# Performance work log

Hardware: AMD Instinct MI355X
Metric: run time of the kernel (lower is better)

Reference implementation:

```python
import jax, jax.numpy as jnp
import numpy as np

NUM_HEADS = 16
HEAD_SIZE = 64
EMB = NUM_HEADS * HEAD_SIZE
B, S = 2, 2048


def setup_inputs() -> dict:
    key = jax.random.key(0)
    ks = jax.random.split(key, 8)
    return {
        "values": jax.random.normal(ks[0], (B, S, EMB), dtype=jnp.float32),
        "keys": jax.random.normal(ks[1], (B, S, EMB), dtype=jnp.float32),
        "queries": jax.random.normal(ks[2], (B, S, EMB), dtype=jnp.float32),
        "mask": jnp.ones((B, 1, 1, S), dtype=jnp.int32),
        "Wq": jax.random.normal(ks[3], (HEAD_SIZE, HEAD_SIZE), dtype=jnp.float32) / np.sqrt(HEAD_SIZE),
        "Wk": jax.random.normal(ks[4], (HEAD_SIZE, HEAD_SIZE), dtype=jnp.float32) / np.sqrt(HEAD_SIZE),
        "Wv": jax.random.normal(ks[5], (HEAD_SIZE, HEAD_SIZE), dtype=jnp.float32) / np.sqrt(HEAD_SIZE),
        "Wout": jax.random.normal(ks[6], (EMB, EMB), dtype=jnp.float32) / np.sqrt(EMB),
        "bout": jax.random.normal(ks[7], (EMB,), dtype=jnp.float32) * 0.01,
    }


def reference(values, keys, queries, mask, Wq, Wk, Wv, Wout, bout):
    n, q_len, E = queries.shape
    H, D = NUM_HEADS, HEAD_SIZE
    # split heads: [n, len, H, D]
    v = values.reshape(n, -1, H, D)
    k = keys.reshape(n, -1, H, D)
    q = queries.reshape(n, q_len, H, D)
    # per-head shared linears (torch Linear: x @ W.T), no bias
    v = jnp.einsum("nkhd,cd->nkhc", v, Wv)
    k = jnp.einsum("nkhd,cd->nkhc", k, Wk)
    q = jnp.einsum("nqhd,cd->nqhc", q, Wq)
    # scores: [n, H, q, k]
    energy = jnp.einsum("nqhd,nkhd->nhqk", q, k)
    energy = jnp.where(mask == 0, jnp.float32(-1e28), energy)
    # NOTE: source scales by sqrt(embedding_size), not head_size
    attn = jax.nn.softmax(energy / jnp.sqrt(jnp.float32(E)), axis=3)
    out = jnp.einsum("nhqk,nkhd->nqhd", attn, v).reshape(n, q_len, E)
    return out @ Wout.T + bout
```

## Files before the change

### kernel.cpp

```cpp
#include <hip/hip_runtime.h>
#include <hip/hip_bf16.h>


#define NHB 16
#define HS  64
#define EMB 1024
#define BB  2
#define SS  2048
#define NT  (SS / 64)

typedef __bf16 bf16_t;
typedef bf16_t bf16x8 __attribute__((ext_vector_type(8)));
typedef bf16_t bf16x4 __attribute__((ext_vector_type(4)));
typedef float  f32x4  __attribute__((ext_vector_type(4)));

__device__ __forceinline__ f32x4 mfma16(bf16x8 a, bf16x8 b, f32x4 c) {
    return __builtin_amdgcn_mfma_f32_16x16x32_bf16(a, b, c, 0, 0, 0);
}

__device__ __forceinline__ float fast_exp2(float x) {
#if __has_builtin(__builtin_amdgcn_exp2f)
    return __builtin_amdgcn_exp2f(x);
#else
    float r;
    asm("v_exp_f32 %0, %1" : "=v"(r) : "v"(x));
    return r;
#endif
}

__global__ __launch_bounds__(512) void proj_kernel(
    const float* __restrict__ queries, const float* __restrict__ keys,
    const float* __restrict__ values,
    const float* __restrict__ Wq, const float* __restrict__ Wk,
    const float* __restrict__ Wv,
    bf16_t* __restrict__ Qb, bf16_t* __restrict__ Kb, bf16_t* __restrict__ Vt)
{
    __shared__ bf16_t Ws[3][64][72];
    __shared__ bf16_t Xs[128][72];

    const int tid  = threadIdx.x;
    const int wave = tid >> 6, lane = tid & 63;
    const int q4 = lane >> 4, l16 = lane & 15;
    const int s0 = blockIdx.x * 128;
    const int h  = blockIdx.y, n = blockIdx.z;

    #pragma unroll
    for (int i = 0; i < 6; ++i) {
        int g = i * 512 + tid;
        int mW = g >> 10;
        int idx4 = g & 1023;
        const float* wp = (mW == 0) ? Wq : (mW == 1) ? Wk : Wv;
        float4 v = ((const float4*)wp)[idx4];
        int r = idx4 >> 4, c = (idx4 & 15) * 4;
        Ws[mW][r][c+0] = (bf16_t)v.x; Ws[mW][r][c+1] = (bf16_t)v.y;
        Ws[mW][r][c+2] = (bf16_t)v.z; Ws[mW][r][c+3] = (bf16_t)v.w;
    }

    const size_t headBase = (size_t)(n * NHB + h) * SS * HS;

    float4 gx[4];
    auto loadX = [&](const float* xp) {
        #pragma unroll
        for (int i = 0; i < 4; ++i) {
            int idx4 = i * 512 + tid;
            int r = idx4 >> 4, c = (idx4 & 15) * 4;
            gx[i] = *(const float4*)&xp[((size_t)(n * SS + s0 + r)) * EMB + h * HS + c];
        }
    };
    loadX(queries);

    for (int p = 0; p < 3; ++p) {
        __syncthreads();
        #pragma unroll
        for (int i = 0; i < 4; ++i) {
            int idx4 = i * 512 + tid;
            int r = idx4 >> 4, c = (idx4 & 15) * 4;
            Xs[r][c+0] = (bf16_t)gx[i].x; Xs[r][c+1] = (bf16_t)gx[i].y;
            Xs[r][c+2] = (bf16_t)gx[i].z; Xs[r][c+3] = (bf16_t)gx[i].w;
        }
        if (p == 0) loadX(keys);
        else if (p == 1) loadX(values);
        __syncthreads();

        bf16x8 xf[2], wf[4][2];
        #pragma unroll
        for (int kk = 0; kk < 2; ++kk)
            xf[kk] = *(const bf16x8*)&Xs[wave * 16 + l16][kk * 32 + q4 * 8];
        #pragma unroll
        for (int ct = 0; ct < 4; ++ct)
            #pragma unroll
            for (int kk = 0; kk < 2; ++kk)
                wf[ct][kk] = *(const bf16x8*)&Ws[p][ct * 16 + l16][kk * 32 + q4 * 8];

        if (p < 2) {
            bf16_t* dst = (p == 0) ? Qb : Kb;
            const float sc = (p == 0) ? (0.03125f * 1.44269504f) : 1.0f;
            bf16x8 lo, hi;
            #pragma unroll
            for (int ct = 0; ct < 4; ++ct) {
                f32x4 acc = {};
                acc = mfma16(wf[ct][0], xf[0], acc);
                acc = mfma16(wf[ct][1], xf[1], acc);
                #pragma unroll
                for (int i = 0; i < 4; ++i) {
                    bf16_t v = (bf16_t)(acc[i] * sc);
                    if (ct < 2) lo[ct * 4 + i] = v;
                    else        hi[(ct - 2) * 4 + i] = v;
                }
            }
            bf16_t* rp = dst + headBase
                + (size_t)(s0 + wave * 16 + l16) * HS + q4 * 16;
            *(bf16x8*)rp = lo;
            *(bf16x8*)(rp + 8) = hi;
        } else {
            #pragma unroll
            for (int ct = 0; ct < 4; ++ct) {
                f32x4 acc = {};
                acc = mfma16(xf[0], wf[ct][0], acc);
                acc = mfma16(xf[1], wf[ct][1], acc);
                bf16x4 pk;
                #pragma unroll
                for (int i = 0; i < 4; ++i) pk[i] = (bf16_t)acc[i];
                *(bf16x4*)&Vt[headBase + (size_t)(ct * 16 + l16) * SS
                              + s0 + (wave >> 1) * 32 + q4 * 8 + (wave & 1) * 4] = pk;
            }
        }
    }
}

__global__ __launch_bounds__(512) void attn_kernel(
    const bf16_t* __restrict__ Qb, const bf16_t* __restrict__ Kb,
    const bf16_t* __restrict__ Vt, const int* __restrict__ mask,
    bf16_t* __restrict__ Og)
{
    __shared__ __align__(16) unsigned char smem[37376];
    auto Ks = (bf16_t(*)[64][72])(smem);
    auto Vs = (bf16_t(*)[64][72])(smem + 18432);
    auto Ms = (float(*)[64])(smem + 36864);
    float* fbuf = (float*)smem;
    float* lbuf = (float*)(smem + 32768);

    const int tid = threadIdx.x;
    const int w = tid >> 6, lane = tid & 63;
    const int q4 = lane >> 4, l16 = lane & 15;
    const int wq = w & 3, wk = w >> 2;
    const int qt = blockIdx.x, h = blockIdx.y, n = blockIdx.z;
    const size_t headBase = (size_t)(n * NHB + h) * SS * HS;
    const int* mrow = mask + n * SS;

    const int sr = tid >> 3, sc = (tid & 7) * 8;
    const bf16_t* kb_src = Kb + headBase + (size_t)sr * HS + sc;
    const bf16_t* vt_src = Vt + headBase + (size_t)sr * SS + sc;

    bf16x8 bq[2][2];
    #pragma unroll
    for (int st = 0; st < 2; ++st) {
        const bf16_t* qptr = Qb + headBase
            + (size_t)(qt * 128 + wq * 32 + st * 16 + l16) * HS;
        bq[st][0] = *(const bf16x8*)&qptr[q4 * 8];
        bq[st][1] = *(const bf16x8*)&qptr[32 + q4 * 8];
    }

    bf16x8 ones;
    #pragma unroll
    for (int i = 0; i < 8; ++i) ones[i] = (bf16_t)1.0f;

    f32x4 oaccT[2][4] = {};
    f32x4 lacc[2] = {};

    *(bf16x8*)&Ks[0][sr][sc] = *(const bf16x8*)kb_src;
    *(bf16x8*)&Vs[0][sr][sc] = *(const bf16x8*)vt_src;
    if (tid < 64) Ms[0][tid] = mrow[tid] ? 0.0f : -3e38f;
    __syncthreads();

    for (int kt = 0; kt < NT; ++kt) {
        const int cur = kt & 1;
        const bool has_next = (kt + 1) < NT;
        bf16x8 gk, gv; float gm = 0.f;
        if (has_next) {
            const int k0n = (kt + 1) * 64;
            gk = *(const bf16x8*)(kb_src + (size_t)k0n * HS);
            gv = *(const bf16x8*)(vt_src + k0n);
            if (tid < 64) gm = mrow[k0n + tid] ? 0.0f : -3e38f;
        }

        f32x4 sacc[2][2];
        #pragma unroll
        for (int c2 = 0; c2 < 2; ++c2) {
            const int ct = wk * 2 + c2;
            float4 bias = *(const float4*)&Ms[cur][ct * 16 + q4 * 4];
            f32x4 b4 = {bias.x, bias.y, bias.z, bias.w};
            sacc[0][c2] = b4; sacc[1][c2] = b4;
            bf16x8 ak0 = *(const bf16x8*)&Ks[cur][ct * 16 + l16][q4 * 8];
            bf16x8 ak1 = *(const bf16x8*)&Ks[cur][ct * 16 + l16][32 + q4 * 8];
            #pragma unroll
            for (int st = 0; st < 2; ++st) {
                sacc[st][c2] = mfma16(ak0, bq[st][0], sacc[st][c2]);
                sacc[st][c2] = mfma16(ak1, bq[st][1], sacc[st][c2]);
            }
        }

        bf16x4 pv[2][2];
        #pragma unroll
        for (int c2 = 0; c2 < 2; ++c2)
            #pragma unroll
            for (int st = 0; st < 2; ++st) {
                bf16x4 pk;
                #pragma unroll
                for (int j = 0; j < 4; ++j)
                    pk[j] = (bf16_t)fast_exp2(sacc[st][c2][j]);
                pv[st][c2] = pk;
            }

        bf16x8 pa[2];
        #pragma unroll
        for (int st = 0; st < 2; ++st)
            pa[st] = __builtin_shufflevector(pv[st][0], pv[st][1],
                                             0, 1, 2, 3, 4, 5, 6, 7);
        #pragma unroll
        for (int dt = 0; dt < 4; ++dt) {
            bf16x8 av = *(const bf16x8*)&Vs[cur][dt * 16 + l16][wk * 32 + q4 * 8];
            oaccT[0][dt] = mfma16(av, pa[0], oaccT[0][dt]);
            oaccT[1][dt] = mfma16(av, pa[1], oaccT[1][dt]);
        }
        lacc[0] = mfma16(ones, pa[0], lacc[0]);
        lacc[1] = mfma16(ones, pa[1], lacc[1]);

        if (has_next) {
            const int nxt = 1 - cur;
            *(bf16x8*)&Ks[nxt][sr][sc] = gk;
            *(bf16x8*)&Vs[nxt][sr][sc] = gv;
            if (tid < 64) Ms[nxt][tid] = gm;
        }
        __syncthreads();
    }

    float ls[2] = {lacc[0][0], lacc[1][0]};

    if (w >= 4) {
        const int lanecol = wq * 64 + lane;
        #pragma unroll
        for (int st = 0; st < 2; ++st) {
            #pragma unroll
            for (int dt = 0; dt < 4; ++dt)
                #pragma unroll
                for (int j = 0; j < 4; ++j)
                    fbuf[(st * 16 + dt * 4 + j) * 256 + lanecol] = oaccT[st][dt][j];
            lbuf[st * 256 + lanecol] = ls[st];
        }
    }
    __syncthreads();
    if (w < 4) {
        const int lanecol = wq * 64 + lane;
        #pragma unroll
        for (int st = 0; st < 2; ++st) {
            #pragma unroll
            for (int dt = 0; dt < 4; ++dt)
                #pragma unroll
                for (int j = 0; j < 4; ++j)
                    oaccT[st][dt][j] += fbuf[(st * 16 + dt * 4 + j) * 256 + lanecol];
            ls[st] += lbuf[st * 256 + lanecol];
        }
        #pragma unroll
        for (int st = 0; st < 2; ++st) {
            const float inv = 1.f / ls[st];
            const int qrow = qt * 128 + wq * 32 + st * 16 + l16;
            bf16_t* obase = Og + ((size_t)(n * SS + qrow)) * EMB + h * HS;
            #pragma unroll
            for (int dt = 0; dt < 4; ++dt) {
                bf16x4 ov;
                #pragma unroll
                for (int j = 0; j < 4; ++j) ov[j] = (bf16_t)(oaccT[st][dt][j] * inv);
                *(bf16x4*)&obase[dt * 16 + q4 * 4] = ov;
            }
        }
    }
}

__global__ __launch_bounds__(512) void outproj_kernel(
    const bf16_t* __restrict__ Og, const float* __restrict__ Wout,
    const float* __restrict__ bout, float* __restrict__ out)
{
    __shared__ bf16_t As[2][128][72];
    __shared__ bf16_t Bs[2][64][72];
    const int tid = threadIdx.x;
    const int w = tid >> 6, lane = tid & 63;
    const int q4 = lane >> 4, l16 = lane & 15;
    const int wr = w >> 1, wc = w & 1;
    const int t0 = blockIdx.x * 128, c0 = blockIdx.y * 64;

    const int sr0 = tid >> 3, sc0 = (tid & 7) * 8;
    const int sr1 = sr0 + 64;
    const bf16_t* a0 = Og + (size_t)(t0 + sr0) * EMB + sc0;
    const bf16_t* a1 = Og + (size_t)(t0 + sr1) * EMB + sc0;
    const float*  b0 = Wout + (size_t)(c0 + sr0) * EMB + sc0;

    auto cvt8 = [](float4 x, float4 y) {
        bf16x8 r;
        r[0] = (bf16_t)x.x; r[1] = (bf16_t)x.y; r[2] = (bf16_t)x.z; r[3] = (bf16_t)x.w;
        r[4] = (bf16_t)y.x; r[5] = (bf16_t)y.y; r[6] = (bf16_t)y.z; r[7] = (bf16_t)y.w;
        return r;
    };

    f32x4 acc[2][2] = {};

    *(bf16x8*)&As[0][sr0][sc0] = *(const bf16x8*)a0;
    *(bf16x8*)&As[0][sr1][sc0] = *(const bf16x8*)a1;
    *(bf16x8*)&Bs[0][sr0][sc0] = cvt8(*(const float4*)b0, *(const float4*)(b0 + 4));
    __syncthreads();

    const int NE = EMB / 64;
    for (int et = 0; et < NE; ++et) {
        const int cur = et & 1;
        const bool has_next = (et + 1) < NE;
        bf16x8 ga0, ga1; float4 gb0, gb1;
        if (has_next) {
            const int e0 = (et + 1) * 64;
            ga0 = *(const bf16x8*)(a0 + e0); ga1 = *(const bf16x8*)(a1 + e0);
            gb0 = *(const float4*)(b0 + e0); gb1 = *(const float4*)(b0 + e0 + 4);
        }

        bf16x8 af[2][2], bfr[2][2];
        #pragma unroll
        for (int st = 0; st < 2; ++st)
            #pragma unroll
            for (int kk = 0; kk < 2; ++kk)
                af[st][kk] = *(const bf16x8*)&As[cur][wr * 32 + st * 16 + l16][kk * 32 + q4 * 8];
        #pragma unroll
        for (int ct = 0; ct < 2; ++ct)
            #pragma unroll
            for (int kk = 0; kk < 2; ++kk)
                bfr[ct][kk] = *(const bf16x8*)&Bs[cur][wc * 32 + ct * 16 + l16][kk * 32 + q4 * 8];
        #pragma unroll
        for (int st = 0; st < 2; ++st)
            #pragma unroll
            for (int ct = 0; ct < 2; ++ct) {
                acc[st][ct] = mfma16(af[st][0], bfr[ct][0], acc[st][ct]);
                acc[st][ct] = mfma16(af[st][1], bfr[ct][1], acc[st][ct]);
            }

        if (has_next) {
            const int nxt = 1 - cur;
            *(bf16x8*)&As[nxt][sr0][sc0] = ga0;
            *(bf16x8*)&As[nxt][sr1][sc0] = ga1;
            *(bf16x8*)&Bs[nxt][sr0][sc0] = cvt8(gb0, gb1);
        }
        __syncthreads();
    }

    #pragma unroll
    for (int ct = 0; ct < 2; ++ct) {
        const int c = c0 + wc * 32 + ct * 16 + l16;
        const float bias = bout[c];
        #pragma unroll
        for (int st = 0; st < 2; ++st)
            #pragma unroll
            for (int i = 0; i < 4; ++i)
                out[(size_t)(t0 + wr * 32 + st * 16 + q4 * 4 + i) * EMB + c]
                    = acc[st][ct][i] + bias;
    }
}

extern "C" void kernel_launch(void* const* d_in, const int* in_sizes, int n_in,
                              void* d_out, int out_size, void* d_ws, size_t ws_size,
                              hipStream_t stream)
{
    const float* values  = (const float*)d_in[0];
    const float* keys    = (const float*)d_in[1];
    const float* queries = (const float*)d_in[2];
    const int*   mask    = (const int*)d_in[3];
    const float* Wq      = (const float*)d_in[4];
    const float* Wk      = (const float*)d_in[5];
    const float* Wv      = (const float*)d_in[6];
    const float* Wout    = (const float*)d_in[7];
    const float* bout    = (const float*)d_in[8];
    float* out = (float*)d_out;

    const size_t M8 = 8ull * 1024 * 1024;
    bf16_t* Qb = (bf16_t*)d_ws;
    bf16_t* Kb = (bf16_t*)((char*)d_ws + 1 * M8);
    bf16_t* Vt = (bf16_t*)((char*)d_ws + 2 * M8);
    bf16_t* Og = (bf16_t*)((char*)d_ws + 3 * M8);

    proj_kernel<<<dim3(SS / 128, NHB, BB), 512, 0, stream>>>(
        queries, keys, values, Wq, Wk, Wv, Qb, Kb, Vt);
    attn_kernel<<<dim3(SS / 128, NHB, BB), 512, 0, stream>>>(
        Qb, Kb, Vt, mask, Og);
    outproj_kernel<<<dim3((BB * SS) / 128, EMB / 64), 512, 0, stream>>>(
        Og, Wout, bout, out);
}
```

Baseline: 169.1 us.

## Load projection inputs directly to registers and pre-convert Wout for wider out-projection tiles

The projection kernel now loads each wave's Q/K/V input rows straight into MFMA fragment registers as bf16, which removes the shared-memory staging buffer and its per-pass barriers. A separate kernel converts Wout to bf16 once into workspace that aliases the Qb buffer, which is already consumed by then. The out-projection kernel uses 128x128 tiles with K-step 32, loads bf16 directly for both operands, and stores float4 rows with the bias added. The trade-offs are an extra kernel launch, more accumulators per wave, and a dependency on the workspace-aliasing order being safe.

```diff
diff --git a/kernel.cpp b/kernel.cpp
--- a/kernel.cpp
+++ b/kernel.cpp
@@ -28,7 +28,14 @@
 #endif
 }
 
-__global__ __launch_bounds__(512) void proj_kernel(
+__device__ __forceinline__ bf16x8 cvt8f(float4 x, float4 y) {
+    bf16x8 r;
+    r[0] = (bf16_t)x.x; r[1] = (bf16_t)x.y; r[2] = (bf16_t)x.z; r[3] = (bf16_t)x.w;
+    r[4] = (bf16_t)y.x; r[5] = (bf16_t)y.y; r[6] = (bf16_t)y.z; r[7] = (bf16_t)y.w;
+    return r;
+}
+
+__global__ __launch_bounds__(512, 4) void proj_kernel(
     const float* __restrict__ queries, const float* __restrict__ keys,
     const float* __restrict__ values,
     const float* __restrict__ Wq, const float* __restrict__ Wk,
@@ -36,7 +43,6 @@
     bf16_t* __restrict__ Qb, bf16_t* __restrict__ Kb, bf16_t* __restrict__ Vt)
 {
     __shared__ bf16_t Ws[3][64][72];
-    __shared__ bf16_t Xs[128][72];
 
     const int tid  = threadIdx.x;
     const int wave = tid >> 6, lane = tid & 63;
@@ -56,36 +62,27 @@
         Ws[mW][r][c+2] = (bf16_t)v.z; Ws[mW][r][c+3] = (bf16_t)v.w;
     }
 
+    const size_t xrow = (size_t)(n * SS + s0 + wave * 16 + l16) * EMB + h * HS;
+    const float* xsrc[3] = {queries, keys, values};
+    bf16x8 xb[3][2];
+    #pragma unroll
+    for (int p = 0; p < 3; ++p) {
+        const float* rp = xsrc[p] + xrow;
+        float4 t0 = *(const float4*)(rp + q4 * 8);
+        float4 t1 = *(const float4*)(rp + q4 * 8 + 4);
+        float4 t2 = *(const float4*)(rp + 32 + q4 * 8);
+        float4 t3 = *(const float4*)(rp + 32 + q4 * 8 + 4);
+        xb[p][0] = cvt8f(t0, t1);
+        xb[p][1] = cvt8f(t2, t3);
+    }
+
+    __syncthreads();
+
     const size_t headBase = (size_t)(n * NHB + h) * SS * HS;
 
-    float4 gx[4];
-    auto loadX = [&](const float* xp) {
-        #pragma unroll
-        for (int i = 0; i < 4; ++i) {
-            int idx4 = i * 512 + tid;
-            int r = idx4 >> 4, c = (idx4 & 15) * 4;
-            gx[i] = *(const float4*)&xp[((size_t)(n * SS + s0 + r)) * EMB + h * HS + c];
-        }
-    };
-    loadX(queries);
-
+    #pragma unroll
     for (int p = 0; p < 3; ++p) {
-        __syncthreads();
-        #pragma unroll
-        for (int i = 0; i < 4; ++i) {
-            int idx4 = i * 512 + tid;
-            int r = idx4 >> 4, c = (idx4 & 15) * 4;
-            Xs[r][c+0] = (bf16_t)gx[i].x; Xs[r][c+1] = (bf16_t)gx[i].y;
-            Xs[r][c+2] = (bf16_t)gx[i].z; Xs[r][c+3] = (bf16_t)gx[i].w;
-        }
-        if (p == 0) loadX(keys);
-        else if (p == 1) loadX(values);
-        __syncthreads();
-
-        bf16x8 xf[2], wf[4][2];
-        #pragma unroll
-        for (int kk = 0; kk < 2; ++kk)
-            xf[kk] = *(const bf16x8*)&Xs[wave * 16 + l16][kk * 32 + q4 * 8];
+        bf16x8 wf[4][2];
         #pragma unroll
         for (int ct = 0; ct < 4; ++ct)
             #pragma unroll
@@ -99,8 +96,8 @@
             #pragma unroll
             for (int ct = 0; ct < 4; ++ct) {
                 f32x4 acc = {};
-                acc = mfma16(wf[ct][0], xf[0], acc);
-                acc = mfma16(wf[ct][1], xf[1], acc);
+                acc = mfma16(wf[ct][0], xb[p][0], acc);
+                acc = mfma16(wf[ct][1], xb[p][1], acc);
                 #pragma unroll
                 for (int i = 0; i < 4; ++i) {
                     bf16_t v = (bf16_t)(acc[i] * sc);
@@ -116,8 +113,8 @@
             #pragma unroll
             for (int ct = 0; ct < 4; ++ct) {
                 f32x4 acc = {};
-                acc = mfma16(xf[0], wf[ct][0], acc);
-                acc = mfma16(xf[1], wf[ct][1], acc);
+                acc = mfma16(xb[2][0], wf[ct][0], acc);
+                acc = mfma16(xb[2][1], wf[ct][1], acc);
                 bf16x4 pk;
                 #pragma unroll
                 for (int i = 0; i < 4; ++i) pk[i] = (bf16_t)acc[i];
@@ -277,87 +274,81 @@
     }
 }
 
+__global__ __launch_bounds__(256) void wcvt_kernel(
+    const float* __restrict__ W, bf16_t* __restrict__ Wb)
+{
+    const int idx = blockIdx.x * 256 + threadIdx.x;
+    float4 a = ((const float4*)W)[idx * 2];
+    float4 b = ((const float4*)W)[idx * 2 + 1];
+    *(bf16x8*)&Wb[idx * 8] = cvt8f(a, b);
+}
+
 __global__ __launch_bounds__(512) void outproj_kernel(
-    const bf16_t* __restrict__ Og, const float* __restrict__ Wout,
+    const bf16_t* __restrict__ Og, const bf16_t* __restrict__ Wb,
     const float* __restrict__ bout, float* __restrict__ out)
 {
-    __shared__ bf16_t As[2][128][72];
-    __shared__ bf16_t Bs[2][64][72];
+    __shared__ bf16_t As[2][128][40];
+    __shared__ bf16_t Bs[2][128][40];
+
     const int tid = threadIdx.x;
     const int w = tid >> 6, lane = tid & 63;
     const int q4 = lane >> 4, l16 = lane & 15;
-    const int wr = w >> 1, wc = w & 1;
-    const int t0 = blockIdx.x * 128, c0 = blockIdx.y * 64;
-
-    const int sr0 = tid >> 3, sc0 = (tid & 7) * 8;
-    const int sr1 = sr0 + 64;
-    const bf16_t* a0 = Og + (size_t)(t0 + sr0) * EMB + sc0;
-    const bf16_t* a1 = Og + (size_t)(t0 + sr1) * EMB + sc0;
-    const float*  b0 = Wout + (size_t)(c0 + sr0) * EMB + sc0;
-
-    auto cvt8 = [](float4 x, float4 y) {
-        bf16x8 r;
-        r[0] = (bf16_t)x.x; r[1] = (bf16_t)x.y; r[2] = (bf16_t)x.z; r[3] = (bf16_t)x.w;
-        r[4] = (bf16_t)y.x; r[5] = (bf16_t)y.y; r[6] = (bf16_t)y.z; r[7] = (bf16_t)y.w;
-        return r;
-    };
-
-    f32x4 acc[2][2] = {};
-
-    *(bf16x8*)&As[0][sr0][sc0] = *(const bf16x8*)a0;
-    *(bf16x8*)&As[0][sr1][sc0] = *(const bf16x8*)a1;
-    *(bf16x8*)&Bs[0][sr0][sc0] = cvt8(*(const float4*)b0, *(const float4*)(b0 + 4));
+    const int wr = w >> 2, wc = w & 3;
+    const int t0 = blockIdx.x * 128, c0 = blockIdx.y * 128;
+
+    const int sr = tid >> 2, sc = (tid & 3) * 8;
+    const bf16_t* asrc = Og + (size_t)(t0 + sr) * EMB + sc;
+    const bf16_t* bsrc = Wb + (size_t)(c0 + sr) * EMB + sc;
+
+    f32x4 acc[4][2] = {};
+
+    *(bf16x8*)&As[0][sr][sc] = *(const bf16x8*)asrc;
+    *(bf16x8*)&Bs[0][sr][sc] = *(const bf16x8*)bsrc;
     __syncthreads();
 
-    const int NE = EMB / 64;
+    const int NE = EMB / 32;
     for (int et = 0; et < NE; ++et) {
         const int cur = et & 1;
         const bool has_next = (et + 1) < NE;
-        bf16x8 ga0, ga1; float4 gb0, gb1;
+        bf16x8 ga, gb;
         if (has_next) {
-            const int e0 = (et + 1) * 64;
-            ga0 = *(const bf16x8*)(a0 + e0); ga1 = *(const bf16x8*)(a1 + e0);
-            gb0 = *(const float4*)(b0 + e0); gb1 = *(const float4*)(b0 + e0 + 4);
-        }
-
-        bf16x8 af[2][2], bfr[2][2];
-        #pragma unroll
-        for (int st = 0; st < 2; ++st)
-            #pragma unroll
-            for (int kk = 0; kk < 2; ++kk)
-                af[st][kk] = *(const bf16x8*)&As[cur][wr * 32 + st * 16 + l16][kk * 32 + q4 * 8];
+            const int e0 = (et + 1) * 32;
+            ga = *(const bf16x8*)(asrc + e0);
+            gb = *(const bf16x8*)(bsrc + e0);
+        }
+
+        bf16x8 af[4], bfr[2];
+        #pragma unroll
+        for (int st = 0; st < 4; ++st)
+            af[st] = *(const bf16x8*)&As[cur][wr * 64 + st * 16 + l16][q4 * 8];
         #pragma unroll
         for (int ct = 0; ct < 2; ++ct)
-            #pragma unroll
-            for (int kk = 0; kk < 2; ++kk)
-                bfr[ct][kk] = *(const bf16x8*)&Bs[cur][wc * 32 + ct * 16 + l16][kk * 32 + q4 * 8];
-        #pragma unroll
-        for (int st = 0; st < 2; ++st)
-            #pragma unroll
-            for (int ct = 0; ct < 2; ++ct) {
-                acc[st][ct] = mfma16(af[st][0], bfr[ct][0], acc[st][ct]);
-                acc[st][ct] = mfma16(af[st][1], bfr[ct][1], acc[st][ct]);
-            }
+            bfr[ct] = *(const bf16x8*)&Bs[cur][wc * 32 + ct * 16 + l16][q4 * 8];
+        #pragma unroll
+        for (int st = 0; st < 4; ++st)
+            #pragma unroll
+            for (int ct = 0; ct < 2; ++ct)
+                acc[st][ct] = mfma16(bfr[ct], af[st], acc[st][ct]);
 
         if (has_next) {
             const int nxt = 1 - cur;
-            *(bf16x8*)&As[nxt][sr0][sc0] = ga0;
-            *(bf16x8*)&As[nxt][sr1][sc0] = ga1;
-            *(bf16x8*)&Bs[nxt][sr0][sc0] = cvt8(gb0, gb1);
+            *(bf16x8*)&As[nxt][sr][sc] = ga;
+            *(bf16x8*)&Bs[nxt][sr][sc] = gb;
         }
         __syncthreads();
     }
 
     #pragma unroll
-    for (int ct = 0; ct < 2; ++ct) {
-        const int c = c0 + wc * 32 + ct * 16 + l16;
-        const float bias = bout[c];
-        #pragma unroll
-        for (int st = 0; st < 2; ++st)
-            #pragma unroll
-            for (int i = 0; i < 4; ++i)
-                out[(size_t)(t0 + wr * 32 + st * 16 + q4 * 4 + i) * EMB + c]
-                    = acc[st][ct][i] + bias;
+    for (int st = 0; st < 4; ++st) {
+        const int t = t0 + wr * 64 + st * 16 + l16;
+        float* orow = out + (size_t)t * EMB + c0 + wc * 32;
+        #pragma unroll
+        for (int ct = 0; ct < 2; ++ct) {
+            const float4 bb = *(const float4*)&bout[c0 + wc * 32 + ct * 16 + q4 * 4];
+            float4 v = {acc[st][ct][0] + bb.x, acc[st][ct][1] + bb.y,
+                        acc[st][ct][2] + bb.z, acc[st][ct][3] + bb.w};
+            *(float4*)&orow[ct * 16 + q4 * 4] = v;
+        }
     }
 }
 
@@ -381,11 +372,13 @@
     bf16_t* Kb = (bf16_t*)((char*)d_ws + 1 * M8);
     bf16_t* Vt = (bf16_t*)((char*)d_ws + 2 * M8);
     bf16_t* Og = (bf16_t*)((char*)d_ws + 3 * M8);
+    bf16_t* Wb = (bf16_t*)d_ws;
 
     proj_kernel<<<dim3(SS / 128, NHB, BB), 512, 0, stream>>>(
         queries, keys, values, Wq, Wk, Wv, Qb, Kb, Vt);
     attn_kernel<<<dim3(SS / 128, NHB, BB), 512, 0, stream>>>(
         Qb, Kb, Vt, mask, Og);
-    outproj_kernel<<<dim3((BB * SS) / 128, EMB / 64), 512, 0, stream>>>(
-        Og, Wout, bout, out);
-}
+    wcvt_kernel<<<dim3(512), 256, 0, stream>>>(Wout, Wb);
+    outproj_kernel<<<dim3((BB * SS) / 128, EMB / 128), 512, 0, stream>>>(
+        Og, Wb, bout, out);
+}
```

Result: slower. 175.7 us (+3.9%).

## Halve attention block to 4 waves with 64 query rows each, remap grid

Applied to the files above, without the earlier changes.

The attention kernel now runs 256-thread blocks of 4 waves instead of 8, and each wave handles 64 query rows instead of 32. This doubles reuse of each K/V fragment read from shared memory across more MFMAs. The grid is flattened to 512 blocks with a swizzled mapping so that blocks sharing a head are scheduled close together for L2 reuse. The change also adds s_setprio around the MFMA sections and gives the cross-wave reduction a padded row-major buffer layout. In exchange, per-thread register use grows and fewer waves are available to hide latency.

```diff
diff --git a/kernel.cpp b/kernel.cpp
--- a/kernel.cpp
+++ b/kernel.cpp
@@ -128,7 +128,7 @@
     }
 }
 
-__global__ __launch_bounds__(512) void attn_kernel(
+__global__ __launch_bounds__(256) void attn_kernel(
     const bf16_t* __restrict__ Qb, const bf16_t* __restrict__ Kb,
     const bf16_t* __restrict__ Vt, const int* __restrict__ mask,
     bf16_t* __restrict__ Og)
@@ -138,25 +138,31 @@
     auto Vs = (bf16_t(*)[64][72])(smem + 18432);
     auto Ms = (float(*)[64])(smem + 36864);
     float* fbuf = (float*)smem;
-    float* lbuf = (float*)(smem + 32768);
+    float* lbuf = (float*)(smem + 34816);
 
     const int tid = threadIdx.x;
     const int w = tid >> 6, lane = tid & 63;
     const int q4 = lane >> 4, l16 = lane & 15;
-    const int wq = w & 3, wk = w >> 2;
-    const int qt = blockIdx.x, h = blockIdx.y, n = blockIdx.z;
+    const int wq = w & 1, wk = w >> 1;
+
+    const int bid = blockIdx.x;
+    const int r = bid & 7, t = bid >> 3;
+    const int gi = t >> 4, qt = t & 15;
+    const int g = gi * 8 + r;
+    const int h = g & 15, n = g >> 4;
+
     const size_t headBase = (size_t)(n * NHB + h) * SS * HS;
     const int* mrow = mask + n * SS;
 
-    const int sr = tid >> 3, sc = (tid & 7) * 8;
+    const int sr = tid >> 2, sc = (tid & 3) * 16;
     const bf16_t* kb_src = Kb + headBase + (size_t)sr * HS + sc;
     const bf16_t* vt_src = Vt + headBase + (size_t)sr * SS + sc;
 
-    bf16x8 bq[2][2];
+    bf16x8 bq[4][2];
     #pragma unroll
-    for (int st = 0; st < 2; ++st) {
+    for (int st = 0; st < 4; ++st) {
         const bf16_t* qptr = Qb + headBase
-            + (size_t)(qt * 128 + wq * 32 + st * 16 + l16) * HS;
+            + (size_t)(qt * 128 + wq * 64 + st * 16 + l16) * HS;
         bq[st][0] = *(const bf16x8*)&qptr[q4 * 8];
         bq[st][1] = *(const bf16x8*)&qptr[32 + q4 * 8];
     }
@@ -165,106 +171,112 @@
     #pragma unroll
     for (int i = 0; i < 8; ++i) ones[i] = (bf16_t)1.0f;
 
-    f32x4 oaccT[2][4] = {};
-    f32x4 lacc[2] = {};
-
-    *(bf16x8*)&Ks[0][sr][sc] = *(const bf16x8*)kb_src;
-    *(bf16x8*)&Vs[0][sr][sc] = *(const bf16x8*)vt_src;
+    f32x4 oaccT[4][4] = {};
+    f32x4 lacc[4] = {};
+
+    *(bf16x8*)&Ks[0][sr][sc]     = *(const bf16x8*)kb_src;
+    *(bf16x8*)&Ks[0][sr][sc + 8] = *(const bf16x8*)(kb_src + 8);
+    *(bf16x8*)&Vs[0][sr][sc]     = *(const bf16x8*)vt_src;
+    *(bf16x8*)&Vs[0][sr][sc + 8] = *(const bf16x8*)(vt_src + 8);
     if (tid < 64) Ms[0][tid] = mrow[tid] ? 0.0f : -3e38f;
     __syncthreads();
 
     for (int kt = 0; kt < NT; ++kt) {
         const int cur = kt & 1;
         const bool has_next = (kt + 1) < NT;
-        bf16x8 gk, gv; float gm = 0.f;
+        bf16x8 gk0, gk1, gv0, gv1; float gm = 0.f;
         if (has_next) {
             const int k0n = (kt + 1) * 64;
-            gk = *(const bf16x8*)(kb_src + (size_t)k0n * HS);
-            gv = *(const bf16x8*)(vt_src + k0n);
+            gk0 = *(const bf16x8*)(kb_src + (size_t)k0n * HS);
+            gk1 = *(const bf16x8*)(kb_src + (size_t)k0n * HS + 8);
+            gv0 = *(const bf16x8*)(vt_src + k0n);
+            gv1 = *(const bf16x8*)(vt_src + k0n + 8);
             if (tid < 64) gm = mrow[k0n + tid] ? 0.0f : -3e38f;
         }
 
-        f32x4 sacc[2][2];
+        f32x4 sacc[4][2];
+        __builtin_amdgcn_s_setprio(1);
         #pragma unroll
         for (int c2 = 0; c2 < 2; ++c2) {
             const int ct = wk * 2 + c2;
             float4 bias = *(const float4*)&Ms[cur][ct * 16 + q4 * 4];
             f32x4 b4 = {bias.x, bias.y, bias.z, bias.w};
-            sacc[0][c2] = b4; sacc[1][c2] = b4;
             bf16x8 ak0 = *(const bf16x8*)&Ks[cur][ct * 16 + l16][q4 * 8];
             bf16x8 ak1 = *(const bf16x8*)&Ks[cur][ct * 16 + l16][32 + q4 * 8];
             #pragma unroll
-            for (int st = 0; st < 2; ++st) {
-                sacc[st][c2] = mfma16(ak0, bq[st][0], sacc[st][c2]);
-                sacc[st][c2] = mfma16(ak1, bq[st][1], sacc[st][c2]);
-            }
-        }
-
-        bf16x4 pv[2][2];
-        #pragma unroll
-        for (int c2 = 0; c2 < 2; ++c2)
-            #pragma unroll
-            for (int st = 0; st < 2; ++st) {
-                bf16x4 pk;
-                #pragma unroll
-                for (int j = 0; j < 4; ++j)
-                    pk[j] = (bf16_t)fast_exp2(sacc[st][c2][j]);
-                pv[st][c2] = pk;
-            }
-
-        bf16x8 pa[2];
-        #pragma unroll
-        for (int st = 0; st < 2; ++st)
-            pa[st] = __builtin_shufflevector(pv[st][0], pv[st][1],
-                                             0, 1, 2, 3, 4, 5, 6, 7);
+            for (int st = 0; st < 4; ++st) {
+                f32x4 s = mfma16(ak0, bq[st][0], b4);
+                sacc[st][c2] = mfma16(ak1, bq[st][1], s);
+            }
+        }
+        __builtin_amdgcn_s_setprio(0);
+
+        bf16x8 pa[4];
+        #pragma unroll
+        for (int st = 0; st < 4; ++st) {
+            bf16x4 p0, p1;
+            #pragma unroll
+            for (int j = 0; j < 4; ++j) {
+                p0[j] = (bf16_t)fast_exp2(sacc[st][0][j]);
+                p1[j] = (bf16_t)fast_exp2(sacc[st][1][j]);
+            }
+            pa[st] = __builtin_shufflevector(p0, p1, 0, 1, 2, 3, 4, 5, 6, 7);
+        }
+
+        __builtin_amdgcn_s_setprio(1);
         #pragma unroll
         for (int dt = 0; dt < 4; ++dt) {
             bf16x8 av = *(const bf16x8*)&Vs[cur][dt * 16 + l16][wk * 32 + q4 * 8];
-            oaccT[0][dt] = mfma16(av, pa[0], oaccT[0][dt]);
-            oaccT[1][dt] = mfma16(av, pa[1], oaccT[1][dt]);
-        }
-        lacc[0] = mfma16(ones, pa[0], lacc[0]);
-        lacc[1] = mfma16(ones, pa[1], lacc[1]);
+            #pragma unroll
+            for (int st = 0; st < 4; ++st)
+                oaccT[st][dt] = mfma16(av, pa[st], oaccT[st][dt]);
+        }
+        #pragma unroll
+        for (int st = 0; st < 4; ++st)
+            lacc[st] = mfma16(ones, pa[st], lacc[st]);
+        __builtin_amdgcn_s_setprio(0);
 
         if (has_next) {
             const int nxt = 1 - cur;
-            *(bf16x8*)&Ks[nxt][sr][sc] = gk;
-            *(bf16x8*)&Vs[nxt][sr][sc] = gv;
+            *(bf16x8*)&Ks[nxt][sr][sc]     = gk0;
+            *(bf16x8*)&Ks[nxt][sr][sc + 8] = gk1;
+            *(bf16x8*)&Vs[nxt][sr][sc]     = gv0;
+            *(bf16x8*)&Vs[nxt][sr][sc + 8] = gv1;
             if (tid < 64) Ms[nxt][tid] = gm;
         }
         __syncthreads();
     }
 
-    float ls[2] = {lacc[0][0], lacc[1][0]};
-
-    if (w >= 4) {
-        const int lanecol = wq * 64 + lane;
-        #pragma unroll
-        for (int st = 0; st < 2; ++st) {
+    float ls[4] = {lacc[0][0], lacc[1][0], lacc[2][0], lacc[3][0]};
+
+    if (wk == 1) {
+        #pragma unroll
+        for (int st = 0; st < 4; ++st) {
+            const int row = wq * 64 + st * 16 + l16;
             #pragma unroll
             for (int dt = 0; dt < 4; ++dt)
                 #pragma unroll
                 for (int j = 0; j < 4; ++j)
-                    fbuf[(st * 16 + dt * 4 + j) * 256 + lanecol] = oaccT[st][dt][j];
-            lbuf[st * 256 + lanecol] = ls[st];
+                    fbuf[row * 68 + dt * 16 + q4 * 4 + j] = oaccT[st][dt][j];
+            lbuf[row] = ls[st];
         }
     }
     __syncthreads();
-    if (w < 4) {
-        const int lanecol = wq * 64 + lane;
-        #pragma unroll
-        for (int st = 0; st < 2; ++st) {
+    if (wk == 0) {
+        #pragma unroll
+        for (int st = 0; st < 4; ++st) {
+            const int row = wq * 64 + st * 16 + l16;
             #pragma unroll
             for (int dt = 0; dt < 4; ++dt)
                 #pragma unroll
                 for (int j = 0; j < 4; ++j)
-                    oaccT[st][dt][j] += fbuf[(st * 16 + dt * 4 + j) * 256 + lanecol];
-            ls[st] += lbuf[st * 256 + lanecol];
-        }
-        #pragma unroll
-        for (int st = 0; st < 2; ++st) {
+                    oaccT[st][dt][j] += fbuf[row * 68 + dt * 16 + q4 * 4 + j];
+            ls[st] += lbuf[row];
+        }
+        #pragma unroll
+        for (int st = 0; st < 4; ++st) {
             const float inv = 1.f / ls[st];
-            const int qrow = qt * 128 + wq * 32 + st * 16 + l16;
+            const int qrow = qt * 128 + wq * 64 + st * 16 + l16;
             bf16_t* obase = Og + ((size_t)(n * SS + qrow)) * EMB + h * HS;
             #pragma unroll
             for (int dt = 0; dt < 4; ++dt) {
@@ -384,7 +396,7 @@
 
     proj_kernel<<<dim3(SS / 128, NHB, BB), 512, 0, stream>>>(
         queries, keys, values, Wq, Wk, Wv, Qb, Kb, Vt);
-    attn_kernel<<<dim3(SS / 128, NHB, BB), 512, 0, stream>>>(
+    attn_kernel<<<dim3(512), 256, 0, stream>>>(
         Qb, Kb, Vt, mask, Og);
     outproj_kernel<<<dim3((BB * SS) / 128, EMB / 64), 512, 0, stream>>>(
         Og, Wout, bout, out);
```

Measured after the change: 175.0 us. +3.5%, slower.

## Load K fragments directly from global, remap blocks per XCD, add MFMA priority

Applied to the files above, without the earlier changes.

The attention kernel no longer stages K tiles through shared memory. Each wave loads its K MFMA fragments straight from global memory into registers, which removes the K LDS writes and reads and shrinks shared memory. The grid is flattened to 1D with a block-index remap so blocks sharing a head are grouped per XCD (stride 8) for L2 reuse. s_setprio is raised around the MFMA sections. The risk is that the direct global K loads are now exposed latency inside the loop rather than being prefetched one tile ahead.

```diff
diff --git a/kernel.cpp b/kernel.cpp
--- a/kernel.cpp
+++ b/kernel.cpp
@@ -133,10 +133,9 @@
     const bf16_t* __restrict__ Vt, const int* __restrict__ mask,
     bf16_t* __restrict__ Og)
 {
-    __shared__ __align__(16) unsigned char smem[37376];
-    auto Ks = (bf16_t(*)[64][72])(smem);
-    auto Vs = (bf16_t(*)[64][72])(smem + 18432);
-    auto Ms = (float(*)[64])(smem + 36864);
+    __shared__ __align__(16) unsigned char smem[34816];
+    auto Vs = (bf16_t(*)[64][72])(smem);
+    auto Ms = (float(*)[64])(smem + 18432);
     float* fbuf = (float*)smem;
     float* lbuf = (float*)(smem + 32768);
 
@@ -144,13 +143,19 @@
     const int w = tid >> 6, lane = tid & 63;
     const int q4 = lane >> 4, l16 = lane & 15;
     const int wq = w & 3, wk = w >> 2;
-    const int qt = blockIdx.x, h = blockIdx.y, n = blockIdx.z;
+
+    const int bid = blockIdx.x;
+    const int r = bid & 7, t = bid >> 3;
+    const int gi = t >> 4, qt = t & 15;
+    const int g = gi * 8 + r;
+    const int h = g & 15, n = g >> 4;
+
     const size_t headBase = (size_t)(n * NHB + h) * SS * HS;
     const int* mrow = mask + n * SS;
 
     const int sr = tid >> 3, sc = (tid & 7) * 8;
-    const bf16_t* kb_src = Kb + headBase + (size_t)sr * HS + sc;
     const bf16_t* vt_src = Vt + headBase + (size_t)sr * SS + sc;
+    const bf16_t* kb_frag = Kb + headBase + (size_t)l16 * HS + q4 * 8;
 
     bf16x8 bq[2][2];
     #pragma unroll
@@ -168,7 +173,6 @@
     f32x4 oaccT[2][4] = {};
     f32x4 lacc[2] = {};
 
-    *(bf16x8*)&Ks[0][sr][sc] = *(const bf16x8*)kb_src;
     *(bf16x8*)&Vs[0][sr][sc] = *(const bf16x8*)vt_src;
     if (tid < 64) Ms[0][tid] = mrow[tid] ? 0.0f : -3e38f;
     __syncthreads();
@@ -176,29 +180,37 @@
     for (int kt = 0; kt < NT; ++kt) {
         const int cur = kt & 1;
         const bool has_next = (kt + 1) < NT;
-        bf16x8 gk, gv; float gm = 0.f;
+        const int k0 = kt * 64;
+        bf16x8 gv; float gm = 0.f;
         if (has_next) {
-            const int k0n = (kt + 1) * 64;
-            gk = *(const bf16x8*)(kb_src + (size_t)k0n * HS);
+            const int k0n = k0 + 64;
             gv = *(const bf16x8*)(vt_src + k0n);
             if (tid < 64) gm = mrow[k0n + tid] ? 0.0f : -3e38f;
         }
 
+        bf16x8 ak[2][2];
+        #pragma unroll
+        for (int c2 = 0; c2 < 2; ++c2) {
+            const int ct = wk * 2 + c2;
+            const bf16_t* kp = kb_frag + (size_t)(k0 + ct * 16) * HS;
+            ak[c2][0] = *(const bf16x8*)kp;
+            ak[c2][1] = *(const bf16x8*)(kp + 32);
+        }
+
         f32x4 sacc[2][2];
+        __builtin_amdgcn_s_setprio(1);
         #pragma unroll
         for (int c2 = 0; c2 < 2; ++c2) {
             const int ct = wk * 2 + c2;
             float4 bias = *(const float4*)&Ms[cur][ct * 16 + q4 * 4];
             f32x4 b4 = {bias.x, bias.y, bias.z, bias.w};
-            sacc[0][c2] = b4; sacc[1][c2] = b4;
-            bf16x8 ak0 = *(const bf16x8*)&Ks[cur][ct * 16 + l16][q4 * 8];
-            bf16x8 ak1 = *(const bf16x8*)&Ks[cur][ct * 16 + l16][32 + q4 * 8];
             #pragma unroll
             for (int st = 0; st < 2; ++st) {
-                sacc[st][c2] = mfma16(ak0, bq[st][0], sacc[st][c2]);
-                sacc[st][c2] = mfma16(ak1, bq[st][1], sacc[st][c2]);
-            }
-        }
+                f32x4 s = mfma16(ak[c2][0], bq[st][0], b4);
+                sacc[st][c2] = mfma16(ak[c2][1], bq[st][1], s);
+            }
+        }
+        __builtin_amdgcn_s_setprio(0);
 
         bf16x4 pv[2][2];
         #pragma unroll
@@ -217,6 +229,7 @@
         for (int st = 0; st < 2; ++st)
             pa[st] = __builtin_shufflevector(pv[st][0], pv[st][1],
                                              0, 1, 2, 3, 4, 5, 6, 7);
+        __builtin_amdgcn_s_setprio(1);
         #pragma unroll
         for (int dt = 0; dt < 4; ++dt) {
             bf16x8 av = *(const bf16x8*)&Vs[cur][dt * 16 + l16][wk * 32 + q4 * 8];
@@ -225,10 +238,10 @@
         }
         lacc[0] = mfma16(ones, pa[0], lacc[0]);
         lacc[1] = mfma16(ones, pa[1], lacc[1]);
+        __builtin_amdgcn_s_setprio(0);
 
         if (has_next) {
             const int nxt = 1 - cur;
-            *(bf16x8*)&Ks[nxt][sr][sc] = gk;
             *(bf16x8*)&Vs[nxt][sr][sc] = gv;
             if (tid < 64) Ms[nxt][tid] = gm;
         }
@@ -384,7 +397,7 @@
 
     proj_kernel<<<dim3(SS / 128, NHB, BB), 512, 0, stream>>>(
         queries, keys, values, Wq, Wk, Wv, Qb, Kb, Vt);
-    attn_kernel<<<dim3(SS / 128, NHB, BB), 512, 0, stream>>>(
+    attn_kernel<<<dim3(512), 512, 0, stream>>>(
         Qb, Kb, Vt, mask, Og);
     outproj_kernel<<<dim3((BB * SS) / 128, EMB / 64), 512, 0, stream>>>(
         Og, Wout, bout, out);
```

Result: slower. 204.7 us (+21.1%).
